# Optimization experiments

Hardware: AMD Instinct MI355X
Metric: run time of the kernel (lower is better)

## Reference

```python
import jax, jax.numpy as jnp
import numpy as np

N = 100000   # nodes
E = 1000000  # edges
D = 128      # in_dim == out_dim (residual enabled)
EPS = 1e-5   # BatchNorm1d default eps


def setup_inputs() -> dict:
    key = jax.random.key(0)
    k = jax.random.split(key, 5)
    feature = jax.random.normal(k[0], (N, D), dtype=jnp.float32)
    src = jax.random.randint(k[1], (E,), 0, N, dtype=jnp.int32)
    dst = jax.random.randint(k[2], (E,), 0, N, dtype=jnp.int32)
    # nn.Linear(in_dim, out_dim): W is [out, in]
    W = jax.random.normal(k[3], (D, D), dtype=jnp.float32) / np.sqrt(D).astype(np.float32)
    b = jnp.zeros((D,), dtype=jnp.float32)
    gamma = jnp.ones((D,), dtype=jnp.float32)
    beta = jnp.zeros((D,), dtype=jnp.float32)
    return {"feature": feature, "src": src, "dst": dst, "W": W, "b": b,
            "gamma": gamma, "beta": beta}


def reference(feature, src, dst, W, b, gamma, beta):
    # update_all(copy_src('h'), mean): gather src features, mean-reduce onto dst
    deg = jax.ops.segment_sum(jnp.ones((E,), dtype=feature.dtype), dst,
                              num_segments=N)                      # [N]
    agg = jax.ops.segment_sum(feature[src], dst, num_segments=N)   # [N, D]
    agg = agg / jnp.maximum(deg, 1.0)[:, None]  # zero in-degree -> 0 (DGL mean)
    # NodeApplyModule: linear
    h = agg @ W.T + b                                              # [N, D]
    # BatchNorm1d over node dimension (training-mode batch stats, biased var)
    mean = jnp.mean(h, axis=0)
    var = jnp.var(h, axis=0)
    h = (h - mean) * jax.lax.rsqrt(var + EPS) * gamma + beta
    # activation, residual; dropout p=0.0 -> identity
    h = jax.nn.relu(h)
    h = feature + h
    return h
```

## Files before the change

kernel.cpp:

```cpp
#include <hip/hip_runtime.h>

typedef unsigned short u16;
typedef unsigned int u32;

#define D_DIM 128
#define CHUNK 4096
#define NSTRIPE 32
#define LCN 12800

typedef __attribute__((ext_vector_type(8))) short bf16x8;
typedef __attribute__((ext_vector_type(4))) float f32x4;

__device__ __forceinline__ float bf2f(u16 h) {
    u32 u = ((u32)h) << 16;
    return __uint_as_float(u);
}
__device__ __forceinline__ u16 f2bf(float f) {
    u32 u = __float_as_uint(f);
    u32 r = (u >> 16) & 1u;
    u += 0x7fffu + r;
    return (u16)(u >> 16);
}
__device__ __forceinline__ float lo16(u32 u) { return bf2f((u16)(u & 0xffffu)); }
__device__ __forceinline__ float hi16(u32 u) { return bf2f((u16)(u >> 16)); }

__global__ void GCNLayer_76647986365164_kernel(
        int* p, int nwords, const u32* w, int* flag,
        const float* __restrict__ f, u16* __restrict__ fb,
        const void* __restrict__ W, u16* __restrict__ wpre,
        int total8, int zb) {
    const int tid = threadIdx.x;
    const int b = blockIdx.x;
    if (b < zb) {
        int i = b * 256 + tid;
        if (i < nwords) p[i] = 0;
        return;
    }
    __shared__ int cnt;
    if (tid == 0) cnt = 0;
    __syncthreads();
    {
        int c = 0;
        for (int j = 0; j < 4; ++j) {
            u32 x = w[tid * 4 + j];
            u32 e = (x >> 7) & 0xFFu;
            if (e >= 100u && e <= 140u) c++;
        }
        atomicAdd(&cnt, c);
    }
    __syncthreads();
    const int bf = (cnt >= 700) ? 1 : 0;
    if (b == zb && tid == 0) flag[0] = bf;

    if (b == gridDim.x - 1) {
        #pragma unroll
        for (int i = 0; i < 8; ++i) {
            int idx = i * 256 + tid;
            int frag = idx >> 6, dl = idx & 63;
            int ot = frag >> 2, kt = frag & 3;
            int dg = dl >> 4, dc = dl & 15;
            int row = ot * 16 + dc, col = kt * 32 + dg * 8;
            if (bf) {
                *(uint4*)(wpre + (size_t)idx * 8) =
                    *(const uint4*)((const u16*)W + row * 128 + col);
            } else {
                const float* Wf = (const float*)W;
                float4 x = *(const float4*)(Wf + row * 128 + col);
                float4 y = *(const float4*)(Wf + row * 128 + col + 4);
                float v[8] = {x.x, x.y, x.z, x.w, y.x, y.y, y.z, y.w};
                u16 h0[8], h1[8];
                #pragma unroll
                for (int j = 0; j < 8; ++j) {
                    h0[j] = f2bf(v[j]);
                    h1[j] = f2bf(v[j] - bf2f(h0[j]));
                }
                uint4 p0, p1;
                p0.x = (u32)h0[0] | ((u32)h0[1] << 16);
                p0.y = (u32)h0[2] | ((u32)h0[3] << 16);
                p0.z = (u32)h0[4] | ((u32)h0[5] << 16);
                p0.w = (u32)h0[6] | ((u32)h0[7] << 16);
                p1.x = (u32)h1[0] | ((u32)h1[1] << 16);
                p1.y = (u32)h1[2] | ((u32)h1[3] << 16);
                p1.z = (u32)h1[4] | ((u32)h1[5] << 16);
                p1.w = (u32)h1[6] | ((u32)h1[7] << 16);
                *(uint4*)(wpre + (size_t)idx * 8) = p0;
                *(uint4*)(wpre + 16384 + (size_t)idx * 8) = p1;
            }
        }
        return;
    }
    if (bf) return;
    int i = (b - zb) * 256 + tid;
    if (i >= total8) return;
    float4 a = ((const float4*)f)[i * 2];
    float4 bb = ((const float4*)f)[i * 2 + 1];
    uint4 o;
    o.x = (u32)f2bf(a.x) | ((u32)f2bf(a.y) << 16);
    o.y = (u32)f2bf(a.z) | ((u32)f2bf(a.w) << 16);
    o.z = (u32)f2bf(bb.x) | ((u32)f2bf(bb.y) << 16);
    o.w = (u32)f2bf(bb.z) | ((u32)f2bf(bb.w) << 16);
    ((uint4*)fb)[i] = o;
}

__global__ __launch_bounds__(256)
void k_hist(const int* __restrict__ dst, int* __restrict__ cnt,
            int E, int N, int nper, int ES, int P) {
    __shared__ int lc[LCN];
    const int tid = threadIdx.x;
    const int p = blockIdx.x % P;
    const int s = blockIdx.x / P;
    const int lo = p * nper;
    const int hi = min(lo + nper, N);
    const int cn = hi - lo;
    for (int t = tid; t < cn; t += 256) lc[t] = 0;
    __syncthreads();
    const int base = s * ES;
    const int end = min(base + ES, E);
    for (int i = base + tid * 4; i < end; i += 1024) {
        if (i + 3 < end) {
            int4 d4 = *(const int4*)(dst + i);
            if (d4.x >= lo && d4.x < hi) atomicAdd(&lc[d4.x - lo], 1);
            if (d4.y >= lo && d4.y < hi) atomicAdd(&lc[d4.y - lo], 1);
            if (d4.z >= lo && d4.z < hi) atomicAdd(&lc[d4.z - lo], 1);
            if (d4.w >= lo && d4.w < hi) atomicAdd(&lc[d4.w - lo], 1);
        } else {
            for (int k = i; k < end; ++k) {
                int d = dst[k];
                if (d >= lo && d < hi) atomicAdd(&lc[d - lo], 1);
            }
        }
    }
    __syncthreads();
    int* crow = cnt + (size_t)s * N + lo;
    for (int t = tid; t < cn; t += 256) crow[t] = lc[t];
}

__global__ void k_colscan(int* __restrict__ cnt, int* __restrict__ deg, int N) {
    int n = blockIdx.x * 256 + threadIdx.x;
    if (n >= N) return;
    int c[NSTRIPE];
    #pragma unroll
    for (int s = 0; s < NSTRIPE; ++s) c[s] = cnt[(size_t)s * N + n];
    int run = 0;
    #pragma unroll
    for (int s = 0; s < NSTRIPE; ++s) {
        int t = c[s];
        cnt[(size_t)s * N + n] = run;
        run += t;
    }
    deg[n] = run;
}

__global__ void k_scan_local(const int* deg, int* offs, int* bsums, int n) {
    __shared__ int tsum[256];
    const int tid = threadIdx.x;
    const int base = blockIdx.x * CHUNK + tid * 16;
    int v[16];
    int run = 0;
    for (int j = 0; j < 16; ++j) {
        int idx = base + j;
        v[j] = (idx < n) ? deg[idx] : 0;
        run += v[j];
    }
    tsum[tid] = run;
    __syncthreads();
    for (int off = 1; off < 256; off <<= 1) {
        int val = tsum[tid];
        int add = (tid >= off) ? tsum[tid - off] : 0;
        __syncthreads();
        tsum[tid] = val + add;
        __syncthreads();
    }
    int acc = tsum[tid] - run;
    for (int j = 0; j < 16; ++j) {
        int idx = base + j;
        if (idx < n) offs[idx] = acc;
        acc += v[j];
    }
    if (tid == 255) bsums[blockIdx.x] = tsum[255];
}

__global__ void k_scan_add(int* offs, const int* bsums, int n, int nblk) {
    __shared__ int carry_s;
    const int tid = threadIdx.x;
    const int b = blockIdx.x;
    if (tid < 64) {
        int acc = 0;
        for (int k = tid; k < b; k += 64) acc += bsums[k];
        #pragma unroll
        for (int off = 1; off < 64; off <<= 1) acc += __shfl_xor(acc, off);
        if (tid == 0) {
            carry_s = acc;
            if (b == nblk - 1) offs[n] = acc + bsums[b];
        }
    }
    __syncthreads();
    const int carry = carry_s;
    const int base = b * CHUNK + tid * 16;
    for (int j = 0; j < 16; ++j) {
        int idx = base + j;
        if (idx < n) offs[idx] += carry;
    }
}

__global__ __launch_bounds__(256)
void k_scatter(const int* __restrict__ src, const int* __restrict__ dst,
               const int* __restrict__ bases, const int* __restrict__ offs,
               int* __restrict__ csr, int E, int N, int nper, int ES, int P) {
    __shared__ int lc[LCN];
    const int tid = threadIdx.x;
    const int p = blockIdx.x % P;
    const int s = blockIdx.x / P;
    const int lo = p * nper;
    const int hi = min(lo + nper, N);
    const int cn = hi - lo;
    for (int t = tid; t < cn; t += 256) lc[t] = 0;
    __syncthreads();
    const int base = s * ES;
    const int end = min(base + ES, E);
    const int* brow = bases + (size_t)s * N;
    for (int i = base + tid * 4; i < end; i += 1024) {
        if (i + 3 < end) {
            int4 d4 = *(const int4*)(dst + i);
            int4 s4 = *(const int4*)(src + i);
            if (d4.x >= lo && d4.x < hi) {
                int lr = atomicAdd(&lc[d4.x - lo], 1);
                csr[offs[d4.x] + brow[d4.x] + lr] = s4.x;
            }
            if (d4.y >= lo && d4.y < hi) {
                int lr = atomicAdd(&lc[d4.y - lo], 1);
                csr[offs[d4.y] + brow[d4.y] + lr] = s4.y;
            }
            if (d4.z >= lo && d4.z < hi) {
                int lr = atomicAdd(&lc[d4.z - lo], 1);
                csr[offs[d4.z] + brow[d4.z] + lr] = s4.z;
            }
            if (d4.w >= lo && d4.w < hi) {
                int lr = atomicAdd(&lc[d4.w - lo], 1);
                csr[offs[d4.w] + brow[d4.w] + lr] = s4.w;
            }
        } else {
            for (int k = i; k < end; ++k) {
                int d = dst[k];
                if (d >= lo && d < hi) {
                    int lr = atomicAdd(&lc[d - lo], 1);
                    csr[offs[d] + brow[d] + lr] = src[k];
                }
            }
        }
    }
}

__global__ void k_aggregate(const void* feature, const u16* __restrict__ fcopy,
                            const int* offs, const int* csr, u16* agg,
                            const int* flag, int n, int npad) {
    const int tid = threadIdx.x;
    const int node = blockIdx.x * 16 + (tid >> 4);
    const int c = tid & 15;
    if (node >= npad) return;
    const u16* fb = flag[0] ? (const u16*)feature : fcopy;
    const uint4* fq = (const uint4*)fb;
    float acc[8];
    #pragma unroll
    for (int t = 0; t < 8; ++t) acc[t] = 0.f;
    int degn = 0;
    if (node < n) {
        int s = offs[node], e = offs[node + 1];
        degn = e - s;
        for (int j = s; j < e; j += 4) {
            int j1 = j + 1, j2 = j + 2, j3 = j + 3;
            uint4 u0 = {0,0,0,0}, u1 = {0,0,0,0}, u2 = {0,0,0,0}, u3 = {0,0,0,0};
            u0 = fq[(size_t)csr[j] * 16 + c];
            if (j1 < e) u1 = fq[(size_t)csr[j1] * 16 + c];
            if (j2 < e) u2 = fq[(size_t)csr[j2] * 16 + c];
            if (j3 < e) u3 = fq[(size_t)csr[j3] * 16 + c];
            #define ACC8(U) \
                acc[0] += lo16(U.x); acc[1] += hi16(U.x); \
                acc[2] += lo16(U.y); acc[3] += hi16(U.y); \
                acc[4] += lo16(U.z); acc[5] += hi16(U.z); \
                acc[6] += lo16(U.w); acc[7] += hi16(U.w);
            ACC8(u0); ACC8(u1); ACC8(u2); ACC8(u3);
            #undef ACC8
        }
    }
    float sc = 1.0f / (float)(degn > 1 ? degn : 1);
    uint4 o4;
    o4.x = (u32)f2bf(acc[0] * sc) | ((u32)f2bf(acc[1] * sc) << 16);
    o4.y = (u32)f2bf(acc[2] * sc) | ((u32)f2bf(acc[3] * sc) << 16);
    o4.z = (u32)f2bf(acc[4] * sc) | ((u32)f2bf(acc[5] * sc) << 16);
    o4.w = (u32)f2bf(acc[6] * sc) | ((u32)f2bf(acc[7] * sc) << 16);
    ((uint4*)(agg + (size_t)node * D_DIM))[c] = o4;
}

__global__ __launch_bounds__(512, 4)
void k_gemm(u16* __restrict__ agg, const u16* __restrict__ wpre,
            const void* __restrict__ bias, float* __restrict__ parts,
            const int* __restrict__ flag, int n) {
    __shared__ u16 sW[2048 * 8];
    const int tid = threadIdx.x;
    const int rb = blockIdx.x * 128;
    const int bf = flag[0];
    const int w = tid >> 6;
    const int lane = tid & 63;
    const int g = lane >> 4, c = lane & 15;

    bf16x8 afr[4];
    {
        const u16* arow = agg + (size_t)(rb + w * 16 + c) * D_DIM + g * 8;
        #pragma unroll
        for (int kt = 0; kt < 4; ++kt)
            afr[kt] = *(const bf16x8*)(arow + kt * 32);
    }

    f32x4 acc[8];
    #pragma unroll
    for (int ot = 0; ot < 8; ++ot) acc[ot] = (f32x4){0.f, 0.f, 0.f, 0.f};

    const int npass = bf ? 1 : 2;
    for (int pass = 0; pass < npass; ++pass) {
        if (pass) __syncthreads();
        const u16* wsrc = wpre + (size_t)pass * 16384;
        #pragma unroll
        for (int i = 0; i < 4; ++i) {
            int idx = i * 512 + tid;
            *(uint4*)(&sW[idx * 8]) = *(const uint4*)(wsrc + (size_t)idx * 8);
        }
        __syncthreads();
        #pragma unroll
        for (int ot = 0; ot < 8; ++ot) {
            #pragma unroll
            for (int kt = 0; kt < 4; ++kt) {
                bf16x8 bfr = *(const bf16x8*)(&sW[((ot * 4 + kt) * 64 + lane) * 8]);
                acc[ot] = __builtin_amdgcn_mfma_f32_16x16x32_bf16(
                    afr[kt], bfr, acc[ot], 0, 0, 0);
            }
        }
    }

    float* red = (float*)sW;
    __syncthreads();

    const int rowbase = rb + w * 16 + g * 4;
    #pragma unroll
    for (int ot = 0; ot < 8; ++ot) {
        const int o = ot * 16 + c;
        float bv = bf ? bf2f(((const u16*)bias)[o]) : ((const float*)bias)[o];
        float s = 0.f, q = 0.f;
        float hv[4];
        #pragma unroll
        for (int r = 0; r < 4; ++r) {
            float h = acc[ot][r] + bv;
            hv[r] = h;
            if (rowbase + r < n) { s += h; q += h * h; }
        }
        #pragma unroll
        for (int r = 0; r < 4; ++r) {
            float hp = __shfl_xor(hv[r], 1);
            if (!(lane & 1)) {
                u32 pk = (u32)f2bf(hv[r]) | ((u32)f2bf(hp) << 16);
                *(u32*)(agg + (size_t)(rowbase + r) * D_DIM + o) = pk;
            }
        }
        s += __shfl_xor(s, 16); s += __shfl_xor(s, 32);
        q += __shfl_xor(q, 16); q += __shfl_xor(q, 32);
        if (g == 0) { red[w * 256 + o] = s; red[w * 256 + 128 + o] = q; }
    }
    __syncthreads();
    if (tid < 256) {
        float a = 0.f;
        #pragma unroll
        for (int ww = 0; ww < 8; ++ww) a += red[ww * 256 + tid];
        parts[(size_t)blockIdx.x * 256 + tid] = a;
    }
}

__global__ void k_redstats(const float* __restrict__ partials,
                           float* __restrict__ stats, int nb) {
    const int tid = threadIdx.x;
    float a0 = 0.f, a1 = 0.f, a2 = 0.f, a3 = 0.f;
    float a4 = 0.f, a5 = 0.f, a6 = 0.f, a7 = 0.f;
    for (int r0 = blockIdx.x * 8; r0 < nb; r0 += gridDim.x * 8) {
        if (r0 + 0 < nb) a0 += partials[(size_t)(r0 + 0) * 256 + tid];
        if (r0 + 1 < nb) a1 += partials[(size_t)(r0 + 1) * 256 + tid];
        if (r0 + 2 < nb) a2 += partials[(size_t)(r0 + 2) * 256 + tid];
        if (r0 + 3 < nb) a3 += partials[(size_t)(r0 + 3) * 256 + tid];
        if (r0 + 4 < nb) a4 += partials[(size_t)(r0 + 4) * 256 + tid];
        if (r0 + 5 < nb) a5 += partials[(size_t)(r0 + 5) * 256 + tid];
        if (r0 + 6 < nb) a6 += partials[(size_t)(r0 + 6) * 256 + tid];
        if (r0 + 7 < nb) a7 += partials[(size_t)(r0 + 7) * 256 + tid];
    }
    float s = ((a0 + a1) + (a2 + a3)) + ((a4 + a5) + (a6 + a7));
    atomicAdd(&stats[tid], s);
}

__global__ void k_apply(const u16* h, const void* feature, const float* stats,
                        const void* gamma, const void* beta, void* outp,
                        const int* flag, int total8, float invn) {
    __shared__ float ssc[128], ssh[128];
    int tid = threadIdx.x;
    int bf = flag[0];
    if (tid < 128) {
        float mean = stats[tid] * invn;
        float var = stats[128 + tid] * invn - mean * mean;
        var = fmaxf(var, 0.f);
        float inv = rsqrtf(var + 1e-5f);
        float g = bf ? bf2f(((const u16*)gamma)[tid]) : ((const float*)gamma)[tid];
        float bb = bf ? bf2f(((const u16*)beta)[tid]) : ((const float*)beta)[tid];
        float sc = inv * g;
        ssc[tid] = sc;
        ssh[tid] = bb - mean * sc;
    }
    __syncthreads();
    int i = blockIdx.x * 256 + tid;
    if (i >= total8) return;
    size_t base = (size_t)i * 8;
    int c0 = (int)(base & (D_DIM - 1));
    uint4 h4 = ((const uint4*)h)[i];
    u32 hw[4] = {h4.x, h4.y, h4.z, h4.w};
    float hv[8];
    for (int j = 0; j < 4; ++j) { hv[2*j] = lo16(hw[j]); hv[2*j+1] = hi16(hw[j]); }
    float fv[8];
    if (bf) {
        uint4 f4 = ((const uint4*)feature)[i];
        u32 fw[4] = {f4.x, f4.y, f4.z, f4.w};
        for (int j = 0; j < 4; ++j) { fv[2*j] = lo16(fw[j]); fv[2*j+1] = hi16(fw[j]); }
    } else {
        float4 fa = ((const float4*)feature)[i * 2];
        float4 fb = ((const float4*)feature)[i * 2 + 1];
        fv[0]=fa.x; fv[1]=fa.y; fv[2]=fa.z; fv[3]=fa.w;
        fv[4]=fb.x; fv[5]=fb.y; fv[6]=fb.z; fv[7]=fb.w;
    }
    float ov[8];
    for (int j = 0; j < 8; ++j)
        ov[j] = fmaxf(hv[j] * ssc[c0 + j] + ssh[c0 + j], 0.f) + fv[j];
    if (bf) {
        uint4 o4;
        u32 ow[4];
        for (int j = 0; j < 4; ++j)
            ow[j] = (u32)f2bf(ov[2*j]) | ((u32)f2bf(ov[2*j+1]) << 16);
        o4.x = ow[0]; o4.y = ow[1]; o4.z = ow[2]; o4.w = ow[3];
        ((uint4*)outp)[i] = o4;
    } else {
        float4 oa, ob;
        oa.x=ov[0]; oa.y=ov[1]; oa.z=ov[2]; oa.w=ov[3];
        ob.x=ov[4]; ob.y=ov[5]; ob.z=ov[6]; ob.w=ov[7];
        ((float4*)outp)[i * 2] = oa;
        ((float4*)outp)[i * 2 + 1] = ob;
    }
}

static inline size_t al256s(size_t x) { return (x + 255) & ~(size_t)255; }
static inline int gmax1(int x) { return x > 0 ? x : 1; }

extern "C" void kernel_launch(void* const* d_in, const int* in_sizes, int n_in,
                              void* d_out, int out_size, void* d_ws, size_t ws_size,
                              hipStream_t stream) {
    const void* feature = d_in[0];
    const int*  src     = (const int*)d_in[1];
    const int*  dst     = (const int*)d_in[2];
    const void* W       = d_in[3];
    const void* bias    = d_in[4];
    const void* gamma   = d_in[5];
    const void* beta    = d_in[6];

    const int N = in_sizes[0] / D_DIM;
    const int E = in_sizes[1];
    const int Npad = (N + 127) & ~127;
    const int nblk = (N + CHUNK - 1) / CHUNK;
    const int gb   = Npad / 128;

    int P = (N + LCN - 1) / LCN;  if (P < 8) P = 8;
    const int nper = (N + P - 1) / P;
    const int ES = (((E + NSTRIPE - 1) / NSTRIPE) + 3) & ~3;

    char* p = (char*)d_ws;
    size_t o = 0;
    int*   flag   = (int*)(p + o);      o += 256;
    int*   deg    = (int*)(p + o);      o += al256s((size_t)N * 4);
    float* stats  = (float*)(p + o);    o += 256 * 4;
    o = al256s(o);
    u16*   wpre   = (u16*)(p + o);      o += al256s(2 * 16384 * 2);
    int*   bsums  = (int*)(p + o);      o += al256s(((size_t)nblk + 8) * 4);
    int*   offs   = (int*)(p + o);      o += al256s(((size_t)N + 8) * 4);
    int*   csr    = (int*)(p + o);      o += al256s((size_t)E * 4);
    float* parts  = (float*)(p + o);    o += al256s((size_t)gb * 256 * 4);
    u16*   agg    = (u16*)(p + o);      o += al256s((size_t)Npad * D_DIM * 2);
    int*   cnt    = (int*)agg;
    u16*   fbf    = (u16*)d_out;
    (void)ws_size; (void)n_in; (void)out_size;

    int total8 = N * D_DIM / 8;
    int zb = 1;
    int tb = gmax1((total8 + 255) / 256);
    int hblocks = NSTRIPE * P;

    GCNLayer_76647986365164_kernel<<<zb + tb + 1, 256, 0, stream>>>(
        (int*)stats, 256, (const u32*)feature, flag,
        (const float*)feature, fbf, W, wpre, total8, zb);
    k_hist<<<hblocks, 256, 0, stream>>>(dst, cnt, E, N, nper, ES, P);
    k_colscan<<<gmax1((N + 255) / 256), 256, 0, stream>>>(cnt, deg, N);
    k_scan_local<<<gmax1(nblk), 256, 0, stream>>>(deg, offs, bsums, N);
    k_scan_add<<<gmax1(nblk), 256, 0, stream>>>(offs, bsums, N, nblk);
    k_scatter<<<hblocks, 256, 0, stream>>>(src, dst, cnt, offs, csr,
                                           E, N, nper, ES, P);
    k_aggregate<<<gmax1(Npad / 16), 256, 0, stream>>>(
        feature, fbf, offs, csr, agg, flag, N, Npad);
    k_gemm<<<gmax1(gb), 512, 0, stream>>>(agg, wpre, bias, parts, flag, N);
    k_redstats<<<32, 256, 0, stream>>>(parts, stats, gb);
    k_apply<<<gmax1((total8 + 255) / 256), 256, 0, stream>>>(
        agg, feature, stats, gamma, beta, d_out, flag, total8, 1.0f / (float)N);
}
```

Baseline: 319.5 us.

## Double edge stripes and seed scatter counters with precomputed bases

Raises the number of edge stripes from 32 to 64, so the histogram and scatter kernels launch more blocks and each block scans fewer edges. The scatter kernel now seeds its LDS counters with offs plus the per-stripe base. Each atomic then returns the final CSR slot directly, removing two scattered global loads per edge. The column scan reads counts in place rather than staging them in a register array, and the shared agg/cnt buffer is sized to fit the larger count matrix. More stripes also double the count matrix traffic in the histogram and column-scan passes, and every block still reads all of its stripe's edges.

```diff
diff --git a/kernel.cpp b/kernel.cpp
--- a/kernel.cpp
+++ b/kernel.cpp
@@ -5,7 +5,7 @@
 
 #define D_DIM 128
 #define CHUNK 4096
-#define NSTRIPE 32
+#define NSTRIPE 64
 #define LCN 12800
 
 typedef __attribute__((ext_vector_type(8))) short bf16x8;
@@ -138,13 +138,10 @@
 __global__ void k_colscan(int* __restrict__ cnt, int* __restrict__ deg, int N) {
     int n = blockIdx.x * 256 + threadIdx.x;
     if (n >= N) return;
-    int c[NSTRIPE];
-    #pragma unroll
-    for (int s = 0; s < NSTRIPE; ++s) c[s] = cnt[(size_t)s * N + n];
     int run = 0;
     #pragma unroll
     for (int s = 0; s < NSTRIPE; ++s) {
-        int t = c[s];
+        int t = cnt[(size_t)s * N + n];
         cnt[(size_t)s * N + n] = run;
         run += t;
     }
@@ -214,38 +211,24 @@
     const int lo = p * nper;
     const int hi = min(lo + nper, N);
     const int cn = hi - lo;
-    for (int t = tid; t < cn; t += 256) lc[t] = 0;
+    const int* brow = bases + (size_t)s * N;
+    for (int t = tid; t < cn; t += 256)
+        lc[t] = offs[lo + t] + brow[lo + t];
     __syncthreads();
     const int base = s * ES;
     const int end = min(base + ES, E);
-    const int* brow = bases + (size_t)s * N;
     for (int i = base + tid * 4; i < end; i += 1024) {
         if (i + 3 < end) {
             int4 d4 = *(const int4*)(dst + i);
             int4 s4 = *(const int4*)(src + i);
-            if (d4.x >= lo && d4.x < hi) {
-                int lr = atomicAdd(&lc[d4.x - lo], 1);
-                csr[offs[d4.x] + brow[d4.x] + lr] = s4.x;
-            }
-            if (d4.y >= lo && d4.y < hi) {
-                int lr = atomicAdd(&lc[d4.y - lo], 1);
-                csr[offs[d4.y] + brow[d4.y] + lr] = s4.y;
-            }
-            if (d4.z >= lo && d4.z < hi) {
-                int lr = atomicAdd(&lc[d4.z - lo], 1);
-                csr[offs[d4.z] + brow[d4.z] + lr] = s4.z;
-            }
-            if (d4.w >= lo && d4.w < hi) {
-                int lr = atomicAdd(&lc[d4.w - lo], 1);
-                csr[offs[d4.w] + brow[d4.w] + lr] = s4.w;
-            }
+            if (d4.x >= lo && d4.x < hi) csr[atomicAdd(&lc[d4.x - lo], 1)] = s4.x;
+            if (d4.y >= lo && d4.y < hi) csr[atomicAdd(&lc[d4.y - lo], 1)] = s4.y;
+            if (d4.z >= lo && d4.z < hi) csr[atomicAdd(&lc[d4.z - lo], 1)] = s4.z;
+            if (d4.w >= lo && d4.w < hi) csr[atomicAdd(&lc[d4.w - lo], 1)] = s4.w;
         } else {
             for (int k = i; k < end; ++k) {
                 int d = dst[k];
-                if (d >= lo && d < hi) {
-                    int lr = atomicAdd(&lc[d - lo], 1);
-                    csr[offs[d] + brow[d] + lr] = src[k];
-                }
+                if (d >= lo && d < hi) csr[atomicAdd(&lc[d - lo], 1)] = src[k];
             }
         }
     }
@@ -451,6 +434,7 @@
 
 static inline size_t al256s(size_t x) { return (x + 255) & ~(size_t)255; }
 static inline int gmax1(int x) { return x > 0 ? x : 1; }
+static inline size_t smax(size_t a, size_t b) { return a > b ? a : b; }
 
 extern "C" void kernel_launch(void* const* d_in, const int* in_sizes, int n_in,
                               void* d_out, int out_size, void* d_ws, size_t ws_size,
@@ -484,8 +468,10 @@
     int*   offs   = (int*)(p + o);      o += al256s(((size_t)N + 8) * 4);
     int*   csr    = (int*)(p + o);      o += al256s((size_t)E * 4);
     float* parts  = (float*)(p + o);    o += al256s((size_t)gb * 256 * 4);
-    u16*   agg    = (u16*)(p + o);      o += al256s((size_t)Npad * D_DIM * 2);
-    int*   cnt    = (int*)agg;
+    size_t aggBytes = (size_t)Npad * D_DIM * 2;
+    size_t cntBytes = (size_t)NSTRIPE * N * 4;
+    u16*   agg    = (u16*)(p + o);
+    int*   cnt    = (int*)(p + o);      o += al256s(smax(aggBytes, cntBytes));
     u16*   fbf    = (u16*)d_out;
     (void)ws_size; (void)n_in; (void)out_size;
 
```

Result: faster. 281.2 us (-12.0%).
